# Kernel optimization log

Measured on AMD Instinct MI355X. Metric: run time of the kernel, lower is better.

The kernel has to match this reference:

```python
import jax, jax.numpy as jnp
import numpy as np
from jax import lax

B, S, E, SD = 8, 4096, 1024, 8


def setup_inputs() -> dict:
    key = jax.random.key(0)
    ks = jax.random.split(key, 4)
    x = jax.random.normal(ks[0], (B, S, E), dtype=jnp.float32)
    W_in = jax.random.normal(ks[1], (E, E + SD), dtype=jnp.float32) / np.sqrt(E)
    b_in = jnp.zeros((E + SD,), dtype=jnp.float32)
    W_g = jax.random.normal(ks[2], (E + SD, SD), dtype=jnp.float32) / np.sqrt(E + SD)
    b_g = jnp.zeros((SD,), dtype=jnp.float32)
    W_out = jax.random.normal(ks[3], (E + SD, E), dtype=jnp.float32) / np.sqrt(E + SD)
    b_out = jnp.zeros((E,), dtype=jnp.float32)
    return {"x": x, "W_in": W_in, "b_in": b_in, "W_g": W_g, "b_g": b_g,
            "W_out": W_out, "b_out": b_out}


def reference(x, W_in, b_in, W_g, b_g, W_out, b_out):
    embed_dim = W_in.shape[0]
    # State-independent projections batched over the whole sequence.
    combined = jnp.einsum('bse,ec->bsc', x, W_in) + b_in            # [B,S,E+SD]
    embed = combined[..., :embed_dim]                                # [B,S,E]
    state_in = combined[..., embed_dim:]                             # [B,S,SD]
    gate = jax.nn.sigmoid(jnp.einsum('bsc,cd->bsd', combined, W_g) + b_g)  # [B,S,SD]

    # Only the tiny gated state recurrence is sequential.
    def step(state, gs):
        g, si = gs
        new = g * state + (1.0 - g) * si
        return new, new

    state0 = jnp.zeros((x.shape[0], state_in.shape[-1]), dtype=x.dtype)
    g_t = jnp.moveaxis(gate, 1, 0)        # [S,B,SD]
    si_t = jnp.moveaxis(state_in, 1, 0)   # [S,B,SD]
    final_state, states = lax.scan(step, state0, (g_t, si_t))
    states = jnp.moveaxis(states, 0, 1)   # [B,S,SD]

    out = jnp.einsum('bsc,cd->bsd', jnp.concatenate([embed, states], axis=-1), W_out) + b_out
    return out, final_state
```

## Files before the change

kernel.cpp:

```cpp
#include <hip/hip_runtime.h>

typedef unsigned short ushort_t;
typedef __attribute__((ext_vector_type(8))) short short8;
typedef __attribute__((ext_vector_type(4))) float floatx4;

#define B_ 8
#define S_ 4096
#define E_ 1024
#define SD_ 8
#define M_TOTAL (B_ * S_)
#define NC 1032

__device__ __forceinline__ ushort_t f2bf(float f) {
    union { float f; unsigned u; } v; v.f = f;
    unsigned u = v.u;
    unsigned r = (u + 0x7fffu + ((u >> 16) & 1u)) >> 16;
    return (ushort_t)r;
}
__device__ __forceinline__ float bf2f(ushort_t h) {
    union { unsigned u; float f; } v; v.u = ((unsigned)h) << 16;
    return v.f;
}

__device__ __forceinline__ void stage16(ushort_t* lds_base_uniform, const ushort_t* g) {
    __builtin_amdgcn_global_load_lds(
        (const __attribute__((address_space(1))) void*)g,
        (__attribute__((address_space(3))) void*)lds_base_uniform, 16, 0, 0);
}

__global__ __launch_bounds__(256) void prep_ew2(
    const float* __restrict__ W_in, const float* __restrict__ W_out,
    ushort_t* __restrict__ Winb, ushort_t* __restrict__ WoutTa)
{
    const int bid = blockIdx.x, tid = threadIdx.x;
    if (bid < 1024) {
        int i = bid * 256 + tid;
        int k = i >> 8, j0 = (i & 255) * 4;
        float4 v = *(const float4*)(W_in + (size_t)k * NC + j0);
        ushort4 o;
        o.x = f2bf(v.x); o.y = f2bf(v.y); o.z = f2bf(v.z); o.w = f2bf(v.w);
        *(ushort4*)(Winb + (size_t)k * E_ + j0) = o;
    } else {
        int idx = (bid - 1024) * 256 + tid;
        int n = idx >> 10, j = idx & 1023;
        WoutTa[idx] = f2bf(W_out[(size_t)j * E_ + n]);
    }
}


__global__ void wcomb_kernel(const float* __restrict__ W_in, const float* __restrict__ Wg,
                             float* __restrict__ Wc) {
    const int k = blockIdx.x;
    const int lane = threadIdx.x;
    float acc[8] = {0.f,0.f,0.f,0.f,0.f,0.f,0.f,0.f};
    for (int c = lane; c < NC; c += 64) {
        float w = W_in[(size_t)k * NC + c];
#pragma unroll
        for (int d = 0; d < 8; d++) acc[d] += w * Wg[(size_t)c * 8 + d];
    }
#pragma unroll
    for (int d = 0; d < 8; d++) {
#pragma unroll
        for (int off = 32; off >= 1; off >>= 1) acc[d] += __shfl_xor(acc[d], off);
    }
    if (lane == 0) {
#pragma unroll
        for (int d = 0; d < 8; d++) Wc[k * 8 + d] = acc[d];
    }
}

__global__ void prep_small(const float* __restrict__ W_in, const float* __restrict__ Wc,
                           const float* __restrict__ W_out, const float* __restrict__ b_in,
                           const float* __restrict__ Wg, const float* __restrict__ bg,
                           ushort_t* __restrict__ BT16, ushort_t* __restrict__ WoutT2,
                           float* __restrict__ bias16) {
    int idx = blockIdx.x * 256 + threadIdx.x;
    if (idx < 32768) {
        int n = idx >> 10, k = idx & 1023;
        float v;
        if (n < 8)        v = W_in[(size_t)k * NC + 1024 + n];
        else if (n < 16)  v = Wc[k * 8 + (n - 8)];
        else              v = 0.f;
        BT16[idx] = f2bf(v);
    } else {
        int i2 = idx - 32768;
        int n = i2 >> 5, k2 = i2 & 31;
        float v = (k2 < 8) ? W_out[(size_t)(1024 + k2) * E_ + n] : 0.f;
        WoutT2[i2] = f2bf(v);
    }
    if (idx < 32) {
        float s;
        if (idx < 8) s = b_in[1024 + idx];
        else if (idx < 16) {
            int d = idx - 8;
            s = bg[d];
            for (int j = 0; j < NC; j++) s += b_in[j] * Wg[(size_t)j * 8 + d];
        } else s = 0.f;
        bias16[idx] = s;
    }
}

__global__ void bias2_kernel(const float* __restrict__ b_in, const float* __restrict__ W_out,
                             const float* __restrict__ b_out, float* __restrict__ bias2) {
    int n = blockIdx.x * 64 + threadIdx.x;
    float acc = b_out[n];
    for (int j = 0; j < E_; j++) acc += b_in[j] * W_out[(size_t)j * E_ + n];
    bias2[n] = acc;
}

template <bool OUT_BF16, bool EXTRA>
__global__ __launch_bounds__(256, 2) void gemm_bt(
    const ushort_t* __restrict__ A, const ushort_t* __restrict__ BT,
    const ushort_t* __restrict__ A2, const ushort_t* __restrict__ BT2,
    void* __restrict__ Cout, const float* __restrict__ bias,
    int K, int lda, int ldb, int lda2, int ldb2, int ldc)
{
    __shared__ __align__(16) ushort_t sA[128 * 32];
    __shared__ __align__(16) ushort_t sB[128 * 32];
    const int tid = threadIdx.x;
    const int wave = tid >> 6;
    const int lane = tid & 63;

    const int gx = gridDim.x;
    int flat = blockIdx.y * gx + blockIdx.x;
    const int band_size = 8 * gx;
    int band = flat / band_size;
    int r = flat - band * band_size;
    const int m0 = (band * 8 + (r & 7)) * 128;
    const int n0 = (r >> 3) * 128;

    const int wm = wave >> 1, wn = wave & 1;
    const int fr = lane & 15, fq = lane >> 4;
    const int sr = lane >> 2;
    const int sc = (lane & 3) * 8;

    floatx4 acc[4][4];
#pragma unroll
    for (int i = 0; i < 4; i++)
#pragma unroll
        for (int j = 0; j < 4; j++) acc[i][j] = (floatx4)0.f;

    const ushort_t* gA = A + (size_t)(m0 + wave * 32 + sr) * lda + sc;
    const ushort_t* gB = BT + (size_t)(n0 + wave * 32 + sr) * ldb + sc;

    for (int k0 = 0; k0 < K; k0 += 32) {
        __syncthreads();
        stage16(&sA[(wave * 32 + 0) * 32], gA + k0);
        stage16(&sA[(wave * 32 + 16) * 32], gA + (size_t)16 * lda + k0);
        stage16(&sB[(wave * 32 + 0) * 32], gB + k0);
        stage16(&sB[(wave * 32 + 16) * 32], gB + (size_t)16 * ldb + k0);
        __syncthreads();

        short8 a[4], b[4];
#pragma unroll
        for (int i = 0; i < 4; i++)
            a[i] = *(const short8*)&sA[(wm * 64 + i * 16 + fr) * 32 + fq * 8];
#pragma unroll
        for (int j = 0; j < 4; j++)
            b[j] = *(const short8*)&sB[(wn * 64 + j * 16 + fr) * 32 + fq * 8];
#pragma unroll
        for (int i = 0; i < 4; i++)
#pragma unroll
            for (int j = 0; j < 4; j++)
                acc[i][j] = __builtin_amdgcn_mfma_f32_16x16x32_bf16(a[i], b[j], acc[i][j], 0, 0, 0);
    }

    if constexpr (EXTRA) {
        const ushort_t* gA2 = A2 + (size_t)(m0 + wave * 32 + sr) * lda2 + sc;
        const ushort_t* gB2 = BT2 + (size_t)(n0 + wave * 32 + sr) * ldb2 + sc;
        __syncthreads();
        stage16(&sA[(wave * 32 + 0) * 32], gA2);
        stage16(&sA[(wave * 32 + 16) * 32], gA2 + (size_t)16 * lda2);
        stage16(&sB[(wave * 32 + 0) * 32], gB2);
        stage16(&sB[(wave * 32 + 16) * 32], gB2 + (size_t)16 * ldb2);
        __syncthreads();

        short8 a[4], b[4];
#pragma unroll
        for (int i = 0; i < 4; i++)
            a[i] = *(const short8*)&sA[(wm * 64 + i * 16 + fr) * 32 + fq * 8];
#pragma unroll
        for (int j = 0; j < 4; j++)
            b[j] = *(const short8*)&sB[(wn * 64 + j * 16 + fr) * 32 + fq * 8];
#pragma unroll
        for (int i = 0; i < 4; i++)
#pragma unroll
            for (int j = 0; j < 4; j++)
                acc[i][j] = __builtin_amdgcn_mfma_f32_16x16x32_bf16(a[i], b[j], acc[i][j], 0, 0, 0);
    }

#pragma unroll
    for (int i = 0; i < 4; i++) {
        int row = m0 + wm * 64 + i * 16 + fq * 4;
#pragma unroll
        for (int j = 0; j < 4; j++) {
            int col = n0 + wn * 64 + j * 16 + fr;
            float bv = bias ? bias[col] : 0.f;
#pragma unroll
            for (int r2 = 0; r2 < 4; r2++) {
                float v = acc[i][j][r2] + bv;
                if (OUT_BF16)
                    ((ushort_t*)Cout)[(size_t)(row + r2) * ldc + col] = f2bf(v);
                else
                    ((float*)Cout)[(size_t)(row + r2) * ldc + col] = v;
            }
        }
    }
}

__global__ __launch_bounds__(256) void skinny16_cvt(
    const float* __restrict__ X,
    const ushort_t* __restrict__ BT,
    const float* __restrict__ bias,
    ushort_t* __restrict__ xb,
    ushort_t* __restrict__ C)
{
    const int tid = threadIdx.x, wave = tid >> 6, lane = tid & 63;
    const int m0 = blockIdx.x * 16;
    const int fr = lane & 15, fq = lane >> 4;
    const int k0w = wave * 256;

    floatx4 acc = (floatx4)0.f;
    const float*    px  = X  + (size_t)(m0 + fr) * E_ + k0w + fq * 8;
    ushort_t*       pxb = xb + (size_t)(m0 + fr) * E_ + k0w + fq * 8;
    const ushort_t* pb  = BT + (size_t)fr * E_ + k0w + fq * 8;
#pragma unroll
    for (int kk = 0; kk < 256; kk += 32) {
        float4 v0 = *(const float4*)(px + kk);
        float4 v1 = *(const float4*)(px + kk + 4);
        short8 a;
        a[0] = (short)f2bf(v0.x); a[1] = (short)f2bf(v0.y);
        a[2] = (short)f2bf(v0.z); a[3] = (short)f2bf(v0.w);
        a[4] = (short)f2bf(v1.x); a[5] = (short)f2bf(v1.y);
        a[6] = (short)f2bf(v1.z); a[7] = (short)f2bf(v1.w);
        *(short8*)(pxb + kk) = a;
        short8 b0 = *(const short8*)(pb + kk);
        acc = __builtin_amdgcn_mfma_f32_16x16x32_bf16(a, b0, acc, 0, 0, 0);
    }

    __shared__ float red[4][16][16];
#pragma unroll
    for (int r = 0; r < 4; r++) red[wave][fq * 4 + r][fr] = acc[r];
    __syncthreads();
    const int row = tid >> 4, col = tid & 15;
    float v = red[0][row][col] + red[1][row][col] + red[2][row][col] + red[3][row][col]
            + bias[col];
    C[(size_t)(m0 + row) * 32 + col]      = f2bf(v);
    C[(size_t)(m0 + row) * 32 + 16 + col] = (ushort_t)0;
}

__global__ __launch_bounds__(256) void scan_fused(
    ushort_t* __restrict__ comb, float* __restrict__ final_state)
{
    const int b = blockIdx.x >> 3, d = blockIdx.x & 7;
    const int t = threadIdx.x;
    __shared__ float sA[256], sB[256];
    const size_t base = (size_t)b * S_ * 32;
    const int s0 = t * 16;

    float A = 1.f, Bv = 0.f;
    for (int s = s0; s < s0 + 16; s++) {
        size_t m = base + (size_t)s * 32;
        float z = bf2f(comb[m + 8 + d]);
        float g = 1.f / (1.f + __expf(-z));
        float si = bf2f(comb[m + d]);
        Bv = g * Bv + (1.f - g) * si;
        A *= g;
    }
    sA[t] = A; sB[t] = Bv;
    __syncthreads();

    float rA = A, rB = Bv;
    for (int off = 1; off < 256; off <<= 1) {
        float a = 1.f, b_ = 0.f;
        if (t >= off) { a = sA[t - off]; b_ = sB[t - off]; }
        __syncthreads();
        if (t >= off) {
            float nA = a * rA;
            float nB = rA * b_ + rB;
            rA = nA; rB = nB;
        }
        sA[t] = rA; sB[t] = rB;
        __syncthreads();
    }

    float state = (t == 0) ? 0.f : sB[t - 1];
    for (int s = s0; s < s0 + 16; s++) {
        size_t m = base + (size_t)s * 32;
        float z = bf2f(comb[m + 8 + d]);
        float g = 1.f / (1.f + __expf(-z));
        float si = bf2f(comb[m + d]);
        state = g * state + (1.f - g) * si;
        comb[m + d] = f2bf(state);
    }
    if (t == 255) final_state[b * 8 + d] = state;
}

extern "C" void kernel_launch(void* const* d_in, const int* in_sizes, int n_in,
                              void* d_out, int out_size, void* d_ws, size_t ws_size,
                              hipStream_t stream)
{
    (void)in_sizes; (void)n_in; (void)out_size; (void)ws_size;
    const float* x     = (const float*)d_in[0];
    const float* W_in  = (const float*)d_in[1];
    const float* b_in  = (const float*)d_in[2];
    const float* W_g   = (const float*)d_in[3];
    const float* b_g   = (const float*)d_in[4];
    const float* W_out = (const float*)d_in[5];
    const float* b_out = (const float*)d_in[6];

    ushort_t* xb     = (ushort_t*)d_ws;
    ushort_t* comb16 = xb + (size_t)M_TOTAL * E_;
    ushort_t* WbigT  = comb16 + (size_t)M_TOTAL * 32;
    ushort_t* Winb   = WbigT + (size_t)E_ * E_;
    ushort_t* WoutTa = Winb + (size_t)E_ * E_;
    ushort_t* WoutT2 = WoutTa + (size_t)E_ * E_;
    ushort_t* BT16   = WoutT2 + (size_t)E_ * 32;
    float*    Wc     = (float*)(BT16 + (size_t)32 * E_);
    float*    bias16 = Wc + 1024 * 8;
    float*    bias2v = bias16 + 32;

    float* outp = (float*)d_out;
    float* fs = outp + (size_t)M_TOTAL * E_;

    prep_ew2<<<5120, 256, 0, stream>>>(W_in, W_out, Winb, WoutTa);
    wcomb_kernel<<<E_, 64, 0, stream>>>(W_in, W_g, Wc);
    prep_small<<<256, 256, 0, stream>>>(W_in, Wc, W_out, b_in, W_g, b_g, BT16, WoutT2, bias16);
    bias2_kernel<<<E_ / 64, 64, 0, stream>>>(b_in, W_out, b_out, bias2v);

    gemm_bt<true, false><<<dim3(E_ / 128, E_ / 128), 256, 0, stream>>>(
        WoutTa, Winb, nullptr, nullptr, WbigT, nullptr, E_, E_, E_, 0, 0, E_);

    skinny16_cvt<<<M_TOTAL / 16, 256, 0, stream>>>(x, BT16, bias16, xb, comb16);

    scan_fused<<<64, 256, 0, stream>>>(comb16, fs);

    gemm_bt<false, true><<<dim3(E_ / 128, M_TOTAL / 128), 256, 0, stream>>>(
        xb, WbigT, comb16, WoutT2, outp, bias2v, E_, E_, E_, 32, 32, E_);
}
```

Before: 451.0 us.

## Replace main GEMM with 256x256 double-buffered swizzled-LDS kernel over concatenated K

The large output GEMM moves from a 128x128 single-buffered kernel with a separate extra K-step to a new 512-thread 256x256-tile kernel. It stages 64-wide K slices into double-buffered, XOR-swizzled LDS and interleaves the next-slice loads with the MFMA work. The activations and the state columns are packed into one padded K=1152 matrix, and the combined weight is written with matching padding, so the tail step is folded into the main loop. The aim is higher data reuse, overlap of memory and compute, and fewer LDS bank conflicts. In exchange it pads K by 128 (about 12% extra MFMA work), uses 128KB of dynamic LDS, and aliases the temporary weight buffers onto the start of the activation workspace, which relies on launch order.

```diff
diff --git a/kernel.cpp b/kernel.cpp
--- a/kernel.cpp
+++ b/kernel.cpp
@@ -10,6 +10,7 @@
 #define SD_ 8
 #define M_TOTAL (B_ * S_)
 #define NC 1032
+#define KX 1152
 
 __device__ __forceinline__ ushort_t f2bf(float f) {
     union { float f; unsigned u; } v; v.f = f;
@@ -22,15 +23,16 @@
     return v.f;
 }
 
-__device__ __forceinline__ void stage16(ushort_t* lds_base_uniform, const ushort_t* g) {
+__device__ __forceinline__ void gload16(char* lds_uniform, const ushort_t* g) {
     __builtin_amdgcn_global_load_lds(
         (const __attribute__((address_space(1))) void*)g,
-        (__attribute__((address_space(3))) void*)lds_base_uniform, 16, 0, 0);
+        (__attribute__((address_space(3))) void*)lds_uniform, 16, 0, 0);
 }
 
 __global__ __launch_bounds__(256) void prep_ew2(
     const float* __restrict__ W_in, const float* __restrict__ W_out,
-    ushort_t* __restrict__ Winb, ushort_t* __restrict__ WoutTa)
+    ushort_t* __restrict__ Winb, ushort_t* __restrict__ WoutTa,
+    ushort_t* __restrict__ WbigTX)
 {
     const int bid = blockIdx.x, tid = threadIdx.x;
     if (bid < 1024) {
@@ -40,13 +42,17 @@
         ushort4 o;
         o.x = f2bf(v.x); o.y = f2bf(v.y); o.z = f2bf(v.z); o.w = f2bf(v.w);
         *(ushort4*)(Winb + (size_t)k * E_ + j0) = o;
-    } else {
+    } else if (bid < 5120) {
         int idx = (bid - 1024) * 256 + tid;
         int n = idx >> 10, j = idx & 1023;
         WoutTa[idx] = f2bf(W_out[(size_t)j * E_ + n]);
-    }
-}
-
+    } else {
+        int idx = (bid - 5120) * 256 + tid;
+        int n = idx >> 7, c = idx & 127;
+        WbigTX[(size_t)n * KX + 1024 + c] =
+            (c < 8) ? f2bf(W_out[(size_t)(1024 + c) * E_ + n]) : (ushort_t)0;
+    }
+}
 
 __global__ void wcomb_kernel(const float* __restrict__ W_in, const float* __restrict__ Wg,
                              float* __restrict__ Wc) {
@@ -108,12 +114,11 @@
     bias2[n] = acc;
 }
 
-template <bool OUT_BF16, bool EXTRA>
+template <bool OUT_BF16>
 __global__ __launch_bounds__(256, 2) void gemm_bt(
     const ushort_t* __restrict__ A, const ushort_t* __restrict__ BT,
-    const ushort_t* __restrict__ A2, const ushort_t* __restrict__ BT2,
     void* __restrict__ Cout, const float* __restrict__ bias,
-    int K, int lda, int ldb, int lda2, int ldb2, int ldc)
+    int K, int lda, int ldb, int ldc)
 {
     __shared__ __align__(16) ushort_t sA[128 * 32];
     __shared__ __align__(16) ushort_t sB[128 * 32];
@@ -145,34 +150,10 @@
 
     for (int k0 = 0; k0 < K; k0 += 32) {
         __syncthreads();
-        stage16(&sA[(wave * 32 + 0) * 32], gA + k0);
-        stage16(&sA[(wave * 32 + 16) * 32], gA + (size_t)16 * lda + k0);
-        stage16(&sB[(wave * 32 + 0) * 32], gB + k0);
-        stage16(&sB[(wave * 32 + 16) * 32], gB + (size_t)16 * ldb + k0);
-        __syncthreads();
-
-        short8 a[4], b[4];
-#pragma unroll
-        for (int i = 0; i < 4; i++)
-            a[i] = *(const short8*)&sA[(wm * 64 + i * 16 + fr) * 32 + fq * 8];
-#pragma unroll
-        for (int j = 0; j < 4; j++)
-            b[j] = *(const short8*)&sB[(wn * 64 + j * 16 + fr) * 32 + fq * 8];
-#pragma unroll
-        for (int i = 0; i < 4; i++)
-#pragma unroll
-            for (int j = 0; j < 4; j++)
-                acc[i][j] = __builtin_amdgcn_mfma_f32_16x16x32_bf16(a[i], b[j], acc[i][j], 0, 0, 0);
-    }
-
-    if constexpr (EXTRA) {
-        const ushort_t* gA2 = A2 + (size_t)(m0 + wave * 32 + sr) * lda2 + sc;
-        const ushort_t* gB2 = BT2 + (size_t)(n0 + wave * 32 + sr) * ldb2 + sc;
-        __syncthreads();
-        stage16(&sA[(wave * 32 + 0) * 32], gA2);
-        stage16(&sA[(wave * 32 + 16) * 32], gA2 + (size_t)16 * lda2);
-        stage16(&sB[(wave * 32 + 0) * 32], gB2);
-        stage16(&sB[(wave * 32 + 16) * 32], gB2 + (size_t)16 * ldb2);
+        gload16((char*)&sA[(wave * 32 + 0) * 32], gA + k0);
+        gload16((char*)&sA[(wave * 32 + 16) * 32], gA + (size_t)16 * lda + k0);
+        gload16((char*)&sB[(wave * 32 + 0) * 32], gB + k0);
+        gload16((char*)&sB[(wave * 32 + 16) * 32], gB + (size_t)16 * ldb + k0);
         __syncthreads();
 
         short8 a[4], b[4];
@@ -208,12 +189,138 @@
     }
 }
 
+#define NT 18
+__global__ __launch_bounds__(512, 2) void gemm256(
+    const ushort_t* __restrict__ A, const ushort_t* __restrict__ BT,
+    float* __restrict__ out, const float* __restrict__ bias)
+{
+    extern __shared__ char smem[];
+    const int tid = threadIdx.x;
+    const int w = tid >> 6, lane = tid & 63;
+    const int wm = w >> 2, wn = w & 3;
+    const int fr = lane & 15, fq = lane >> 4;
+
+    int flat = blockIdx.x;
+    int wg = (flat & 7) * 64 + (flat >> 3);
+    const int m0 = (wg >> 2) * 256;
+    const int n0 = (wg & 3) * 256;
+
+    const int w2 = w * 2;
+    const int sr0 = (w2 + 0) * 8 + (lane >> 3);
+    const int sr1 = (w2 + 1) * 8 + (lane >> 3);
+    const int scole = (((lane & 7) * 16) ^ ((lane & 32) ? 32 : 0)) >> 1;
+    const size_t gA0 = (size_t)(m0 + sr0) * KX + scole;
+    const size_t gA1 = (size_t)(m0 + sr1) * KX + scole;
+    const size_t gB0 = (size_t)(n0 + sr0) * KX + scole;
+    const size_t gB1 = (size_t)(n0 + sr1) * KX + scole;
+    const int dstw = w2 * 1024;
+
+    const int axor = ((fr >> 2) & 1) << 5;
+    const int acol0 = (fq * 16) ^ axor;
+    const int acol1 = (64 + fq * 16) ^ axor;
+    const int aRd = wm * 16384 + fr * 128;
+    const int bRd = 65536 + (wn >> 1) * 16384 + ((wn & 1) * 64 + fr) * 128;
+
+    floatx4 acc[8][4];
+#pragma unroll
+    for (int i = 0; i < 8; i++)
+#pragma unroll
+        for (int j = 0; j < 4; j++) acc[i][j] = (floatx4)0.f;
+
+#define STAGE_A(buf, t, h)                                                   \
+    do {                                                                     \
+        char* d = smem + (buf) * 32768 + (h) * 16384 + dstw;                 \
+        gload16(d,        A + gA0 + (size_t)(h) * 128 * KX + (t) * 64);      \
+        gload16(d + 1024, A + gA1 + (size_t)(h) * 128 * KX + (t) * 64);     \
+    } while (0)
+#define STAGE_B(buf, t, h)                                                   \
+    do {                                                                     \
+        char* d = smem + 65536 + (buf) * 32768 + (h) * 16384 + dstw;         \
+        gload16(d,        BT + gB0 + (size_t)(h) * 128 * KX + (t) * 64);     \
+        gload16(d + 1024, BT + gB1 + (size_t)(h) * 128 * KX + (t) * 64);    \
+    } while (0)
+
+    STAGE_A(0, 0, 0); STAGE_A(0, 0, 1);
+    STAGE_B(0, 0, 0); STAGE_B(0, 0, 1);
+
+#pragma unroll 1
+    for (int t = 0; t < NT; t++) {
+        const int bufR = (t & 1) * 32768;
+        const int bufW = ((t + 1) & 1) * 32768;
+        const bool more = (t + 1 < NT);
+
+        if (more) {
+            STAGE_A(bufW / 32768, t + 1, 0);
+            __builtin_amdgcn_sched_barrier(0);
+            asm volatile("s_waitcnt vmcnt(2)" ::: "memory");
+        } else {
+            __builtin_amdgcn_sched_barrier(0);
+            asm volatile("s_waitcnt vmcnt(0)" ::: "memory");
+        }
+        __builtin_amdgcn_sched_barrier(0);
+        __builtin_amdgcn_s_barrier();
+        __builtin_amdgcn_sched_barrier(0);
+
+        short8 b[4][2];
+#pragma unroll
+        for (int j = 0; j < 4; j++) {
+            b[j][0] = *(const short8*)(smem + bufR + bRd + j * 2048 + acol0);
+            b[j][1] = *(const short8*)(smem + bufR + bRd + j * 2048 + acol1);
+        }
+
+#pragma unroll
+        for (int q = 0; q < 4; q++) {
+            short8 a[2][2];
+#pragma unroll
+            for (int i2 = 0; i2 < 2; i2++) {
+                int i = q * 2 + i2;
+                a[i2][0] = *(const short8*)(smem + bufR + aRd + i * 2048 + acol0);
+                a[i2][1] = *(const short8*)(smem + bufR + aRd + i * 2048 + acol1);
+            }
+            __builtin_amdgcn_s_setprio(1);
+#pragma unroll
+            for (int i2 = 0; i2 < 2; i2++)
+#pragma unroll
+                for (int j = 0; j < 4; j++)
+#pragma unroll
+                    for (int kk = 0; kk < 2; kk++)
+                        acc[q * 2 + i2][j] = __builtin_amdgcn_mfma_f32_16x16x32_bf16(
+                            a[i2][kk], b[j][kk], acc[q * 2 + i2][j], 0, 0, 0);
+            __builtin_amdgcn_s_setprio(0);
+            if (more) {
+                if (q == 0) STAGE_A(bufW / 32768, t + 1, 1);
+                else if (q == 1) STAGE_B(bufW / 32768, t + 1, 0);
+                else if (q == 2) STAGE_B(bufW / 32768, t + 1, 1);
+            }
+        }
+
+        __builtin_amdgcn_s_barrier();
+        __builtin_amdgcn_sched_barrier(0);
+    }
+#undef STAGE_A
+#undef STAGE_B
+
+    float bv[4];
+#pragma unroll
+    for (int j = 0; j < 4; j++) bv[j] = bias[n0 + wn * 64 + j * 16 + fr];
+#pragma unroll
+    for (int i = 0; i < 8; i++) {
+        int row = m0 + wm * 128 + i * 16 + fq * 4;
+#pragma unroll
+        for (int j = 0; j < 4; j++) {
+            int col = n0 + wn * 64 + j * 16 + fr;
+#pragma unroll
+            for (int r2 = 0; r2 < 4; r2++)
+                out[(size_t)(row + r2) * E_ + col] = acc[i][j][r2] + bv[j];
+        }
+    }
+}
+
 __global__ __launch_bounds__(256) void skinny16_cvt(
     const float* __restrict__ X,
     const ushort_t* __restrict__ BT,
     const float* __restrict__ bias,
-    ushort_t* __restrict__ xb,
-    ushort_t* __restrict__ C)
+    ushort_t* __restrict__ XC)
 {
     const int tid = threadIdx.x, wave = tid >> 6, lane = tid & 63;
     const int m0 = blockIdx.x * 16;
@@ -222,7 +329,7 @@
 
     floatx4 acc = (floatx4)0.f;
     const float*    px  = X  + (size_t)(m0 + fr) * E_ + k0w + fq * 8;
-    ushort_t*       pxb = xb + (size_t)(m0 + fr) * E_ + k0w + fq * 8;
+    ushort_t*       pxb = XC + (size_t)(m0 + fr) * KX + k0w + fq * 8;
     const ushort_t* pb  = BT + (size_t)fr * E_ + k0w + fq * 8;
 #pragma unroll
     for (int kk = 0; kk < 256; kk += 32) {
@@ -245,25 +352,27 @@
     const int row = tid >> 4, col = tid & 15;
     float v = red[0][row][col] + red[1][row][col] + red[2][row][col] + red[3][row][col]
             + bias[col];
-    C[(size_t)(m0 + row) * 32 + col]      = f2bf(v);
-    C[(size_t)(m0 + row) * 32 + 16 + col] = (ushort_t)0;
+    ushort_t* xr = XC + (size_t)(m0 + row) * KX;
+    xr[1024 + col] = f2bf(v);
+#pragma unroll
+    for (int z = 0; z < 7; z++) xr[1040 + col + 16 * z] = (ushort_t)0;
 }
 
 __global__ __launch_bounds__(256) void scan_fused(
-    ushort_t* __restrict__ comb, float* __restrict__ final_state)
+    ushort_t* __restrict__ XC, float* __restrict__ final_state)
 {
     const int b = blockIdx.x >> 3, d = blockIdx.x & 7;
     const int t = threadIdx.x;
     __shared__ float sA[256], sB[256];
-    const size_t base = (size_t)b * S_ * 32;
+    const size_t base = (size_t)b * S_ * KX;
     const int s0 = t * 16;
 
     float A = 1.f, Bv = 0.f;
     for (int s = s0; s < s0 + 16; s++) {
-        size_t m = base + (size_t)s * 32;
-        float z = bf2f(comb[m + 8 + d]);
+        size_t m = base + (size_t)s * KX;
+        float z = bf2f(XC[m + 1032 + d]);
         float g = 1.f / (1.f + __expf(-z));
-        float si = bf2f(comb[m + d]);
+        float si = bf2f(XC[m + 1024 + d]);
         Bv = g * Bv + (1.f - g) * si;
         A *= g;
     }
@@ -286,12 +395,12 @@
 
     float state = (t == 0) ? 0.f : sB[t - 1];
     for (int s = s0; s < s0 + 16; s++) {
-        size_t m = base + (size_t)s * 32;
-        float z = bf2f(comb[m + 8 + d]);
+        size_t m = base + (size_t)s * KX;
+        float z = bf2f(XC[m + 1032 + d]);
         float g = 1.f / (1.f + __expf(-z));
-        float si = bf2f(comb[m + d]);
+        float si = bf2f(XC[m + 1024 + d]);
         state = g * state + (1.f - g) * si;
-        comb[m + d] = f2bf(state);
+        XC[m + 1024 + d] = f2bf(state);
     }
     if (t == 255) final_state[b * 8 + d] = state;
 }
@@ -309,12 +418,11 @@
     const float* W_out = (const float*)d_in[5];
     const float* b_out = (const float*)d_in[6];
 
-    ushort_t* xb     = (ushort_t*)d_ws;
-    ushort_t* comb16 = xb + (size_t)M_TOTAL * E_;
-    ushort_t* WbigT  = comb16 + (size_t)M_TOTAL * 32;
-    ushort_t* Winb   = WbigT + (size_t)E_ * E_;
-    ushort_t* WoutTa = Winb + (size_t)E_ * E_;
-    ushort_t* WoutT2 = WoutTa + (size_t)E_ * E_;
+    ushort_t* XC     = (ushort_t*)d_ws;
+    ushort_t* Winb   = XC;
+    ushort_t* WoutTa = XC + (size_t)E_ * E_;
+    ushort_t* WbigTX = XC + (size_t)M_TOTAL * KX;
+    ushort_t* WoutT2 = WbigTX + (size_t)E_ * KX;
     ushort_t* BT16   = WoutT2 + (size_t)E_ * 32;
     float*    Wc     = (float*)(BT16 + (size_t)32 * E_);
     float*    bias16 = Wc + 1024 * 8;
@@ -323,18 +431,17 @@
     float* outp = (float*)d_out;
     float* fs = outp + (size_t)M_TOTAL * E_;
 
-    prep_ew2<<<5120, 256, 0, stream>>>(W_in, W_out, Winb, WoutTa);
+    prep_ew2<<<5632, 256, 0, stream>>>(W_in, W_out, Winb, WoutTa, WbigTX);
     wcomb_kernel<<<E_, 64, 0, stream>>>(W_in, W_g, Wc);
     prep_small<<<256, 256, 0, stream>>>(W_in, Wc, W_out, b_in, W_g, b_g, BT16, WoutT2, bias16);
     bias2_kernel<<<E_ / 64, 64, 0, stream>>>(b_in, W_out, b_out, bias2v);
 
-    gemm_bt<true, false><<<dim3(E_ / 128, E_ / 128), 256, 0, stream>>>(
-        WoutTa, Winb, nullptr, nullptr, WbigT, nullptr, E_, E_, E_, 0, 0, E_);
-
-    skinny16_cvt<<<M_TOTAL / 16, 256, 0, stream>>>(x, BT16, bias16, xb, comb16);
-
-    scan_fused<<<64, 256, 0, stream>>>(comb16, fs);
-
-    gemm_bt<false, true><<<dim3(E_ / 128, M_TOTAL / 128), 256, 0, stream>>>(
-        xb, WbigT, comb16, WoutT2, outp, bias2v, E_, E_, E_, 32, 32, E_);
-}
+    gemm_bt<true><<<dim3(E_ / 128, E_ / 128), 256, 0, stream>>>(
+        WoutTa, Winb, WbigTX, nullptr, E_, E_, E_, KX);
+
+    skinny16_cvt<<<M_TOTAL / 16, 256, 0, stream>>>(x, BT16, bias16, XC);
+
+    scan_fused<<<64, 256, 0, stream>>>(XC, fs);
+
+    gemm256<<<512, 512, 131072, stream>>>(XC, WbigTX, outp, bias2v);
+}
```

After: 465.2 us. 1.03x slower.
